# Kernel tuning notes

Measured on AMD Instinct MI355X. Metric: run time of the kernel, lower is better.

Reference implementation:

```python
import jax, jax.numpy as jnp
import numpy as np

NUM_HEADS = 8


def _forward(x, Wq, bq, Wk, bk, Wv, bv, Wo, bo, w1, b1, w2, b2, tau):
    B, S, E = x.shape
    H = NUM_HEADS
    hd = E // H
    scale = hd ** -0.5

    def heads(t):
        return t.reshape(B, S, H, hd).transpose(0, 2, 1, 3)  # [B,H,S,hd]

    q = heads(x @ Wq + bq)
    k = heads(x @ Wk + bk)
    v = heads(x @ Wv + bv)
    s = jnp.einsum('bhqd,bhkd->bhqk', q, k) * scale  # [B,H,S,S]

    # ---- autopoietic transform (vectorized over batch, no mask) ----
    s = jnp.clip(jnp.nan_to_num(s, nan=0.0, posinf=10.0, neginf=-10.0), -15.0, 15.0)
    ma = s.mean(axis=1)  # mean over heads -> [B,S,S]
    eps_safe = 0.05  # clamp(eps=1e-6, 0.05, 0.8)
    sa = jnp.clip(jnp.clip(ma, -8.0, 8.0) * eps_safe, -10.0, 10.0)
    # 1x1 conv on [1,1,S,S] == per-channel scalar scale+bias -> [B,C,S,S]
    hid = jax.nn.relu(jnp.clip(sa[:, None] * w1[None, :, None, None]
                               + b1[None, :, None, None], -5.0, 5.0))
    ap = jnp.clip(jnp.einsum('bcij,c->bij', hid, w2) + b2, -5.0, 5.0)
    taylor = jnp.clip(1.0 + 0.05 * (ap * 50.0), 0.5, 1.5)
    sig = jax.nn.sigmoid(taylor)
    p = jax.nn.softmax(jnp.clip(ma, -10.0, 10.0), axis=-1)
    Hent = -p * jnp.log(p + 1e-6)
    Fm = jax.nn.softmax(3.0 * Hent, axis=-1)
    t = sig * Fm
    eo = jnp.sqrt((ma * ma).sum(axis=(1, 2), keepdims=True)) + 1e-4  # fro norm
    et = jnp.sqrt((t * t).sum(axis=(1, 2), keepdims=True)) + 1e-4
    t = jnp.clip(eo / et, 0.8, 1.2) * t
    tm = t.mean(axis=(1, 2), keepdims=True)
    om = ma.mean(axis=(1, 2), keepdims=True)
    tstd = jnp.sqrt(jnp.clip(((t - tm) ** 2).mean(axis=(1, 2), keepdims=True), 0.01, None))
    ostd = jnp.sqrt(jnp.clip(((ma - om) ** 2).mean(axis=(1, 2), keepdims=True), 0.01, None))
    gd = jnp.clip(ostd / tstd, 0.8, 1.2)
    ar = jnp.clip(jnp.abs(ma).max(axis=(1, 2), keepdims=True), 1.0, 10.0)
    sm = jnp.clip(0.3 / jnp.log1p(ar), 0.1, 0.5)
    st = tm + sm * gd * (t - tm)  # scaled_transform
    ent = Hent.mean(axis=(1, 2), keepdims=True)
    ne = ent / jnp.log(jnp.float32(S))  # normalized entropy (max_entropy = log S)
    rr = 0.4 * (1.0 - jnp.clip(ne, 0.0, 0.4))  # residual ratio (base 0.4, entropy-damped)
    # blend transform back into per-head scores (res_scale = 1.0)
    s = s + rr[:, None] * (st - ma)[:, None]

    attn = jax.nn.softmax(s / tau, axis=-1)
    out = jnp.einsum('bhqk,bhkd->bhqd', attn, v)
    out = out.transpose(0, 2, 1, 3).reshape(B, S, E)
    return out @ Wo + bo


def setup_inputs() -> dict:
    key = jax.random.key(0)
    ks = jax.random.split(key, 8)
    B, S, E, C = 4, 512, 512, 128
    w_scale = 0.02
    return {
        'x': jax.random.normal(ks[0], (B, S, E), dtype=jnp.float32),
        'Wq': jax.random.normal(ks[1], (E, E), dtype=jnp.float32) * w_scale,
        'bq': jnp.zeros((E,), jnp.float32),
        'Wk': jax.random.normal(ks[2], (E, E), dtype=jnp.float32) * w_scale,
        'bk': jnp.zeros((E,), jnp.float32),
        'Wv': jax.random.normal(ks[3], (E, E), dtype=jnp.float32) * w_scale,
        'bv': jnp.zeros((E,), jnp.float32),
        'Wo': jax.random.normal(ks[4], (E, E), dtype=jnp.float32) * w_scale,
        'bo': jnp.zeros((E,), jnp.float32),
        'w1': jax.random.normal(ks[5], (C,), dtype=jnp.float32) * 0.5,
        'b1': jnp.zeros((C,), jnp.float32),
        'w2': jax.random.normal(ks[6], (C,), dtype=jnp.float32) * 0.1,
        'b2': jnp.zeros((1,), jnp.float32),
        'tau': jnp.ones((1,), jnp.float32),
    }


def reference(x, Wq, bq, Wk, bk, Wv, bv, Wo, bo, w1, b1, w2, b2, tau):
    return _forward(x, Wq, bq, Wk, bk, Wv, bv, Wo, bo, w1, b1, w2, b2, tau)
```

## Files before the change

kernel.cpp:

```cpp
#include <hip/hip_runtime.h>
#include <math.h>

#define BB 4
#define SS 512
#define EE 512
#define NH 8
#define HD 64
#define NC 128
#define NTAB 4096

typedef _Float16 f16x8 __attribute__((ext_vector_type(8)));
typedef float f32x4 __attribute__((ext_vector_type(4)));

struct HL { _Float16 h, l; };

__device__ __forceinline__ float clampf(float v, float lo, float hi) {
  return fminf(fmaxf(v, lo), hi);
}
__device__ __forceinline__ HL split16(float x) {
  HL r;
  r.h = (_Float16)x;
  r.l = (_Float16)(x - (float)r.h);
  return r;
}

__device__ __forceinline__ float waveRedSum(float v) {
#pragma unroll
  for (int o = 32; o; o >>= 1) v += __shfl_xor(v, o);
  return v;
}
__device__ __forceinline__ float waveRedMax(float v) {
#pragma unroll
  for (int o = 32; o; o >>= 1) v = fmaxf(v, __shfl_xor(v, o));
  return v;
}
__device__ __forceinline__ float blockRedSum(float v, float* red) {
  int tid = threadIdx.x;
  v = waveRedSum(v);
  __syncthreads();
  if ((tid & 63) == 0) red[tid >> 6] = v;
  __syncthreads();
  return red[0] + red[1] + red[2] + red[3];
}
__device__ __forceinline__ float blockRedMax(float v, float* red) {
  int tid = threadIdx.x;
  v = waveRedMax(v);
  __syncthreads();
  if ((tid & 63) == 0) red[tid >> 6] = v;
  __syncthreads();
  return fmaxf(fmaxf(red[0], red[1]), fmaxf(red[2], red[3]));
}

__global__ __launch_bounds__(256) void k_prep(
    const float* __restrict__ Wq, const float* __restrict__ Wk,
    const float* __restrict__ Wv, const float* __restrict__ Wo,
    _Float16* __restrict__ Wth, _Float16* __restrict__ Wtl) {
  const int j = blockIdx.x;
  const int tid = threadIdx.x;
  const int z = j >> 6;
  const int rem = j & 63;
  const int k0 = (rem & 7) * 64, n0 = (rem >> 3) * 64;
  const float* W = (z == 0) ? Wq : (z == 1) ? Wk : (z == 2) ? Wv : Wo;
  __shared__ float Tt[64][68];
  const int r = tid >> 2, c = (tid & 3) * 16;
#pragma unroll
  for (int jj = 0; jj < 16; jj += 4)
    *(float4*)&Tt[r][c + jj] =
        *(const float4*)(W + (size_t)(k0 + r) * EE + n0 + c + jj);
  __syncthreads();
  f16x8 h0, l0, h1, l1;
#pragma unroll
  for (int jj = 0; jj < 8; ++jj) {
    HL r0 = split16(Tt[c + jj][r]);
    HL r1 = split16(Tt[c + 8 + jj][r]);
    h0[jj] = r0.h; l0[jj] = r0.l;
    h1[jj] = r1.h; l1[jj] = r1.l;
  }
  _Float16* dh = Wth + ((size_t)z * EE + n0 + r) * EE + k0 + c;
  _Float16* dl = Wtl + ((size_t)z * EE + n0 + r) * EE + k0 + c;
  *(f16x8*)dh = h0;
  *(f16x8*)(dh + 8) = h1;
  *(f16x8*)dl = l0;
  *(f16x8*)(dl + 8) = l1;
}

__global__ __launch_bounds__(256) void k_qkv_mfma(
    const float* __restrict__ x,
    const _Float16* __restrict__ Wth, const _Float16* __restrict__ Wtl,
    const float* __restrict__ bq, const float* __restrict__ bk,
    const float* __restrict__ bv, const float* __restrict__ w1,
    const float* __restrict__ b1, const float* __restrict__ w2,
    const float* __restrict__ b2, float* __restrict__ T,
    _Float16* __restrict__ qh,
    _Float16* __restrict__ kh, _Float16* __restrict__ kl,
    _Float16* __restrict__ vth, _Float16* __restrict__ vtl) {
  const int which = blockIdx.z;
  const int tid = threadIdx.x;
  const int wave = tid >> 6, lane = tid & 63;
  const int quad = lane >> 4, l16 = lane & 15;
  const int m0 = blockIdx.y * 64;
  const int n0 = blockIdx.x * 64;
  const _Float16* Bh = Wth + (size_t)which * EE * EE;
  const _Float16* Bl = Wtl + (size_t)which * EE * EE;

  __shared__ __align__(16) char smpool[27648];
  _Float16(*LAh)[72] = (_Float16(*)[72])(smpool);
  _Float16(*LBh)[72] = (_Float16(*)[72])(smpool + 9216);
  _Float16(*LBl)[72] = (_Float16(*)[72])(smpool + 18432);
  float(*TR)[68] = (float(*)[68])(smpool);

  const int sr0 = tid >> 3, sc0 = (tid & 7) * 8;
  const int sr1 = sr0 + 32;

  float4 rx0a = *(const float4*)(x + (size_t)(m0 + sr0) * EE + sc0);
  float4 rx0b = *(const float4*)(x + (size_t)(m0 + sr0) * EE + sc0 + 4);
  float4 rx1a = *(const float4*)(x + (size_t)(m0 + sr1) * EE + sc0);
  float4 rx1b = *(const float4*)(x + (size_t)(m0 + sr1) * EE + sc0 + 4);
  f16x8 rB0h = *(const f16x8*)(Bh + (size_t)(n0 + sr0) * EE + sc0);
  f16x8 rB0l = *(const f16x8*)(Bl + (size_t)(n0 + sr0) * EE + sc0);
  f16x8 rB1h = *(const f16x8*)(Bh + (size_t)(n0 + sr1) * EE + sc0);
  f16x8 rB1l = *(const f16x8*)(Bl + (size_t)(n0 + sr1) * EE + sc0);

  f32x4 acc[4] = {};
  for (int k0 = 0; k0 < EE; k0 += 64) {
    if (k0) __syncthreads();
    {
      float f0[8] = {rx0a.x, rx0a.y, rx0a.z, rx0a.w,
                     rx0b.x, rx0b.y, rx0b.z, rx0b.w};
      float f1[8] = {rx1a.x, rx1a.y, rx1a.z, rx1a.w,
                     rx1b.x, rx1b.y, rx1b.z, rx1b.w};
      f16x8 h0, h1;
#pragma unroll
      for (int j = 0; j < 8; ++j) {
        h0[j] = (_Float16)f0[j];
        h1[j] = (_Float16)f1[j];
      }
      *(f16x8*)&LAh[sr0][sc0] = h0;
      *(f16x8*)&LAh[sr1][sc0] = h1;
    }
    *(f16x8*)&LBh[sr0][sc0] = rB0h;
    *(f16x8*)&LBl[sr0][sc0] = rB0l;
    *(f16x8*)&LBh[sr1][sc0] = rB1h;
    *(f16x8*)&LBl[sr1][sc0] = rB1l;
    __syncthreads();
    if (k0 + 64 < EE) {
      const int kn = k0 + 64;
      rx0a = *(const float4*)(x + (size_t)(m0 + sr0) * EE + kn + sc0);
      rx0b = *(const float4*)(x + (size_t)(m0 + sr0) * EE + kn + sc0 + 4);
      rx1a = *(const float4*)(x + (size_t)(m0 + sr1) * EE + kn + sc0);
      rx1b = *(const float4*)(x + (size_t)(m0 + sr1) * EE + kn + sc0 + 4);
      rB0h = *(const f16x8*)(Bh + (size_t)(n0 + sr0) * EE + kn + sc0);
      rB0l = *(const f16x8*)(Bl + (size_t)(n0 + sr0) * EE + kn + sc0);
      rB1h = *(const f16x8*)(Bh + (size_t)(n0 + sr1) * EE + kn + sc0);
      rB1l = *(const f16x8*)(Bl + (size_t)(n0 + sr1) * EE + kn + sc0);
    }
#pragma unroll
    for (int kk = 0; kk < 64; kk += 32) {
      f16x8 ah = *(const f16x8*)&LAh[wave * 16 + l16][kk + quad * 8];
#pragma unroll
      for (int nt = 0; nt < 4; ++nt) {
        f16x8 bhf = *(const f16x8*)&LBh[nt * 16 + l16][kk + quad * 8];
        f16x8 blf = *(const f16x8*)&LBl[nt * 16 + l16][kk + quad * 8];
        acc[nt] = __builtin_amdgcn_mfma_f32_16x16x32_f16(ah, bhf, acc[nt], 0, 0, 0);
        acc[nt] = __builtin_amdgcn_mfma_f32_16x16x32_f16(ah, blf, acc[nt], 0, 0, 0);
      }
    }
  }
  const float* bias = (which == 0) ? bq : (which == 1) ? bk : bv;
  if (which == 2) {
    __syncthreads();
#pragma unroll
    for (int nt = 0; nt < 4; ++nt) {
      const int dcol = nt * 16 + l16;
      const float bb = bias[n0 + nt * 16 + l16];
#pragma unroll
      for (int r = 0; r < 4; ++r)
        TR[dcol][wave * 16 + quad * 4 + r] = acc[nt][r] + bb;
    }
    __syncthreads();
    const int d = tid >> 2, cc = (tid & 3) * 16;
    const int bh = (m0 >> 9) * NH + (n0 >> 6);
    const int si0 = m0 & 511;
    f16x8 h0, l0, h1, l1;
#pragma unroll
    for (int jj = 0; jj < 8; ++jj) {
      HL r0 = split16(TR[d][cc + jj]);
      HL r1 = split16(TR[d][cc + 8 + jj]);
      h0[jj] = r0.h; l0[jj] = r0.l;
      h1[jj] = r1.h; l1[jj] = r1.l;
    }
    _Float16* dh = vth + ((size_t)bh * HD + d) * SS + si0 + cc;
    _Float16* dl = vtl + ((size_t)bh * HD + d) * SS + si0 + cc;
    *(f16x8*)dh = h0;
    *(f16x8*)(dh + 8) = h1;
    *(f16x8*)dl = l0;
    *(f16x8*)(dl + 8) = l1;
  } else {
    const float postscale = (which == 0) ? 0.125f : 1.0f;
    const int mbase = m0 + wave * 16 + quad * 4;
#pragma unroll
    for (int nt = 0; nt < 4; ++nt) {
      const int col = n0 + nt * 16 + l16;
      const float bb = bias[col];
#pragma unroll
      for (int r = 0; r < 4; ++r) {
        const size_t idx = (size_t)(mbase + r) * EE + col;
        const float val = (acc[nt][r] + bb) * postscale;
        if (which == 0) {
          qh[idx] = (_Float16)val;
        } else {
          HL sp = split16(val);
          kh[idx] = sp.h;
          kl[idx] = sp.l;
        }
      }
    }
    if (which == 0 && blockIdx.x == 0 && blockIdx.y < 17) {
      int idx = blockIdx.y * 256 + tid;
      if (idx <= NTAB) {
        float sa = -0.4f + (float)idx * (0.8f / (float)NTAB);
        float ap = 0.f;
#pragma unroll 4
        for (int c = 0; c < NC; ++c) {
          float h = fminf(fmaxf(sa * w1[c] + b1[c], 0.f), 5.f);
          ap += h * w2[c];
        }
        ap = clampf(ap + b2[0], -5.f, 5.f);
        float tay = clampf(1.0f + 0.05f * (ap * 50.0f), 0.5f, 1.5f);
        T[idx] = 1.0f / (1.0f + expf(-tay));
      }
    }
  }
}

__global__ __launch_bounds__(256) void k_ma_mfma(
    const _Float16* __restrict__ qh,
    const _Float16* __restrict__ kh, const _Float16* __restrict__ kl,
    float* __restrict__ ma) {
  const int tid = threadIdx.x;
  const int wave = tid >> 6, lane = tid & 63;
  const int quad = lane >> 4, l16 = lane & 15;
  const int m0 = blockIdx.y * 64;
  const int n0 = blockIdx.x * 64;
  const _Float16* Bh = kh + (size_t)(m0 >> 9) * SS * EE;
  const _Float16* Bl = kl + (size_t)(m0 >> 9) * SS * EE;

  __shared__ _Float16 LAh[64][72], LBh[64][72], LBl[64][72];

  const int sr0 = tid >> 3, sc0 = (tid & 7) * 8;
  const int sr1 = sr0 + 32;

  f16x8 rA0h = *(const f16x8*)(qh + (size_t)(m0 + sr0) * EE + sc0);
  f16x8 rB0h = *(const f16x8*)(Bh + (size_t)(n0 + sr0) * EE + sc0);
  f16x8 rB0l = *(const f16x8*)(Bl + (size_t)(n0 + sr0) * EE + sc0);
  f16x8 rA1h = *(const f16x8*)(qh + (size_t)(m0 + sr1) * EE + sc0);
  f16x8 rB1h = *(const f16x8*)(Bh + (size_t)(n0 + sr1) * EE + sc0);
  f16x8 rB1l = *(const f16x8*)(Bl + (size_t)(n0 + sr1) * EE + sc0);

  f32x4 acc[4] = {};
  for (int k0 = 0; k0 < EE; k0 += 64) {
    if (k0) __syncthreads();
    *(f16x8*)&LAh[sr0][sc0] = rA0h;
    *(f16x8*)&LBh[sr0][sc0] = rB0h;
    *(f16x8*)&LBl[sr0][sc0] = rB0l;
    *(f16x8*)&LAh[sr1][sc0] = rA1h;
    *(f16x8*)&LBh[sr1][sc0] = rB1h;
    *(f16x8*)&LBl[sr1][sc0] = rB1l;
    __syncthreads();
    if (k0 + 64 < EE) {
      const int kn = k0 + 64;
      rA0h = *(const f16x8*)(qh + (size_t)(m0 + sr0) * EE + kn + sc0);
      rB0h = *(const f16x8*)(Bh + (size_t)(n0 + sr0) * EE + kn + sc0);
      rB0l = *(const f16x8*)(Bl + (size_t)(n0 + sr0) * EE + kn + sc0);
      rA1h = *(const f16x8*)(qh + (size_t)(m0 + sr1) * EE + kn + sc0);
      rB1h = *(const f16x8*)(Bh + (size_t)(n0 + sr1) * EE + kn + sc0);
      rB1l = *(const f16x8*)(Bl + (size_t)(n0 + sr1) * EE + kn + sc0);
    }
#pragma unroll
    for (int kk = 0; kk < 64; kk += 32) {
      f16x8 ah = *(const f16x8*)&LAh[wave * 16 + l16][kk + quad * 8];
#pragma unroll
      for (int nt = 0; nt < 4; ++nt) {
        f16x8 bhf = *(const f16x8*)&LBh[nt * 16 + l16][kk + quad * 8];
        f16x8 blf = *(const f16x8*)&LBl[nt * 16 + l16][kk + quad * 8];
        acc[nt] = __builtin_amdgcn_mfma_f32_16x16x32_f16(ah, bhf, acc[nt], 0, 0, 0);
        acc[nt] = __builtin_amdgcn_mfma_f32_16x16x32_f16(ah, blf, acc[nt], 0, 0, 0);
      }
    }
  }
  const int mbase = m0 + wave * 16 + quad * 4;
#pragma unroll
  for (int nt = 0; nt < 4; ++nt) {
    const int col = n0 + nt * 16 + l16;
#pragma unroll
    for (int r = 0; r < 4; ++r) {
      ma[(size_t)(mbase + r) * SS + col] = acc[nt][r] * 0.125f;
    }
  }
}

__global__ __launch_bounds__(256) void k_rowstat(
    const float* __restrict__ ma, const float* __restrict__ T,
    float* __restrict__ t_un, float* __restrict__ rowred) {
  const int row = blockIdx.x * 4 + (threadIdx.x >> 6);
  const int lane = threadIdx.x & 63;

  const float4* p =
      reinterpret_cast<const float4*>(ma + (size_t)row * SS) + lane * 2;
  float4 u0 = p[0], u1 = p[1];
  float m[8] = {u0.x, u0.y, u0.z, u0.w, u1.x, u1.y, u1.z, u1.w};

  float sma = 0.f, sma2 = 0.f, mabs = 0.f;
#pragma unroll
  for (int e = 0; e < 8; ++e) {
    sma += m[e];
    sma2 += m[e] * m[e];
    mabs = fmaxf(mabs, fabsf(m[e]));
  }
  sma = waveRedSum(sma);
  sma2 = waveRedSum(sma2);
  mabs = waveRedMax(mabs);

  float ex[8], esum = 0.f;
#pragma unroll
  for (int e = 0; e < 8; ++e) {
    ex[e] = expf(clampf(m[e], -10.f, 10.f));
    esum += ex[e];
  }
  esum = waveRedSum(esum);
  float inv = 1.0f / esum;
  float Hv[8], sH = 0.f;
#pragma unroll
  for (int e = 0; e < 8; ++e) {
    float pp = ex[e] * inv;
    Hv[e] = -pp * logf(pp + 1e-6f);
    sH += Hv[e];
  }
  sH = waveRedSum(sH);

  float fx[8], fsum = 0.f;
#pragma unroll
  for (int e = 0; e < 8; ++e) {
    fx[e] = expf(3.0f * Hv[e]);
    fsum += fx[e];
  }
  fsum = waveRedSum(fsum);
  float finv = 1.0f / fsum;

  float t[8], st = 0.f, st2 = 0.f;
#pragma unroll
  for (int e = 0; e < 8; ++e) {
    float sa = clampf(m[e], -8.f, 8.f) * 0.05f;
    float pos = (sa + 0.4f) * ((float)NTAB / 0.8f);
    int idx = (int)pos;
    idx = idx < 0 ? 0 : (idx > NTAB - 1 ? NTAB - 1 : idx);
    float frac = pos - (float)idx;
    float g0 = T[idx], g1 = T[idx + 1];
    float sig = g0 + (g1 - g0) * frac;
    t[e] = sig * fx[e] * finv;
    st += t[e];
    st2 += t[e] * t[e];
  }
  st = waveRedSum(st);
  st2 = waveRedSum(st2);
  {
    float4* tp = reinterpret_cast<float4*>(t_un + (size_t)row * SS) + lane * 2;
    float4 w0 = {t[0], t[1], t[2], t[3]}, w1v = {t[4], t[5], t[6], t[7]};
    tp[0] = w0;
    tp[1] = w1v;
  }
  if (lane == 0) {
    float* rp = rowred + (size_t)row * 8;
    rp[0] = sma; rp[1] = sma2; rp[2] = mabs;
    rp[3] = st;  rp[4] = st2;  rp[5] = sH;
  }
}

__global__ __launch_bounds__(256) void k_av_fused(
    const _Float16* __restrict__ qh,
    const _Float16* __restrict__ kh, const _Float16* __restrict__ kl,
    const float* __restrict__ ma, const float* __restrict__ t_un,
    const float* __restrict__ rowred, const float* __restrict__ tau,
    const _Float16* __restrict__ vth, const _Float16* __restrict__ vtl,
    _Float16* __restrict__ oh) {
  const int bh = blockIdx.y;
  const int b_ = bh >> 3, hh = bh & 7;
  const int m0 = blockIdx.x * 32;
  const int tid = threadIdx.x;
  const int wave = tid >> 6, lane = tid & 63;
  const int quad = lane >> 4, l16 = lane & 15;
  const int mt = wave >> 1, nt = wave & 1;

  __shared__ float red[4];
  float c0, c1, c2;
  {
    const float* r0 = rowred + ((size_t)b_ * SS + tid * 2) * 8;
    const float* r1 = r0 + 8;
    float sma = blockRedSum(r0[0] + r1[0], red);
    float sma2 = blockRedSum(r0[1] + r1[1], red);
    float mabs = blockRedMax(fmaxf(r0[2], r1[2]), red);
    float st = blockRedSum(r0[3] + r1[3], red);
    float st2 = blockRedSum(r0[4] + r1[4], red);
    float sH = blockRedSum(r0[5] + r1[5], red);
    const float N = (float)(SS * SS);
    float eo = sqrtf(sma2) + 1e-4f;
    float et = sqrtf(st2) + 1e-4f;
    float r = clampf(eo / et, 0.8f, 1.2f);
    float tmean = r * st / N;
    float om = sma / N;
    float vart = r * r * fmaxf(st2 / N - (st / N) * (st / N), 0.f);
    float tstd = sqrtf(fmaxf(vart, 0.01f));
    float varo = fmaxf(sma2 / N - om * om, 0.f);
    float ostd = sqrtf(fmaxf(varo, 0.01f));
    float gd = clampf(ostd / tstd, 0.8f, 1.2f);
    float ar = clampf(mabs, 1.f, 10.f);
    float sm = clampf(0.3f / log1pf(ar), 0.1f, 0.5f);
    float ent = sH / N;
    float ne = ent / logf((float)SS);
    float rr = 0.4f * (1.f - clampf(ne, 0.f, 0.4f));
    float G = sm * gd;
    c0 = rr * (1.f - G) * tmean;
    c1 = rr * G * r;
    c2 = rr;
  }
  const float itau = 1.0f / tau[0];

  __shared__ _Float16 Ph[32][40];
  __shared__ float Zp[32][2];

  const size_t qbase = (size_t)(b_ * SS + m0 + mt * 16 + l16) * EE + hh * HD;
  f16x8 a_hi[2];
#pragma unroll
  for (int ks = 0; ks < 2; ++ks)
    a_hi[ks] = *(const f16x8*)(qh + qbase + ks * 32 + quad * 8);

  const size_t kbase = (size_t)b_ * SS * EE + hh * HD;
  const size_t vbase = ((size_t)bh * HD + wave * 16 + l16) * SS;
  const size_t mbase =
      (size_t)(b_ * SS + m0 + mt * 16 + quad * 4) * SS + nt * 16 + l16;

  f16x8 kb_h[2], kb_l[2], vb_h, vb_l;
  float mv[4], tv[4];
  {
    const size_t kr = kbase + (size_t)(nt * 16 + l16) * EE;
#pragma unroll
    for (int ks = 0; ks < 2; ++ks) {
      kb_h[ks] = *(const f16x8*)(kh + kr + ks * 32 + quad * 8);
      kb_l[ks] = *(const f16x8*)(kl + kr + ks * 32 + quad * 8);
    }
    vb_h = *(const f16x8*)(vth + vbase + quad * 8);
    vb_l = *(const f16x8*)(vtl + vbase + quad * 8);
#pragma unroll
    for (int r = 0; r < 4; ++r) {
      mv[r] = ma[mbase + (size_t)r * SS];
      tv[r] = t_un[mbase + (size_t)r * SS];
    }
  }

  float z[4] = {0.f, 0.f, 0.f, 0.f};
  f32x4 oacc[2] = {};
  for (int k0 = 0; k0 < SS; k0 += 32) {
    f32x4 qacc = {};
#pragma unroll
    for (int ks = 0; ks < 2; ++ks) {
      qacc = __builtin_amdgcn_mfma_f32_16x16x32_f16(a_hi[ks], kb_h[ks], qacc, 0, 0, 0);
      qacc = __builtin_amdgcn_mfma_f32_16x16x32_f16(a_hi[ks], kb_l[ks], qacc, 0, 0, 0);
    }
    const f16x8 vh_c = vb_h, vl_c = vb_l;
    __syncthreads();
#pragma unroll
    for (int r = 0; r < 4; ++r) {
      float sc = clampf(qacc[r], -15.f, 15.f);
      float v = (sc + c0 + c1 * tv[r] - c2 * mv[r]) * itau;
      float e = expf(v) * 1.52587890625e-05f;
      z[r] += e;
      Ph[mt * 16 + quad * 4 + r][nt * 16 + l16] = (_Float16)e;
    }
    if (k0 + 32 < SS) {
      const int kn = k0 + 32;
      const size_t kr = kbase + (size_t)(kn + nt * 16 + l16) * EE;
#pragma unroll
      for (int ks = 0; ks < 2; ++ks) {
        kb_h[ks] = *(const f16x8*)(kh + kr + ks * 32 + quad * 8);
        kb_l[ks] = *(const f16x8*)(kl + kr + ks * 32 + quad * 8);
      }
      vb_h = *(const f16x8*)(vth + vbase + kn + quad * 8);
      vb_l = *(const f16x8*)(vtl + vbase + kn + quad * 8);
#pragma unroll
      for (int r = 0; r < 4; ++r) {
        mv[r] = ma[mbase + (size_t)r * SS + kn];
        tv[r] = t_un[mbase + (size_t)r * SS + kn];
      }
    }
    __syncthreads();
#pragma unroll
    for (int mt2 = 0; mt2 < 2; ++mt2) {
      f16x8 ah = *(const f16x8*)&Ph[mt2 * 16 + l16][quad * 8];
      oacc[mt2] = __builtin_amdgcn_mfma_f32_16x16x32_f16(ah, vh_c, oacc[mt2], 0, 0, 0);
      oacc[mt2] = __builtin_amdgcn_mfma_f32_16x16x32_f16(ah, vl_c, oacc[mt2], 0, 0, 0);
    }
  }
#pragma unroll
  for (int off = 1; off < 16; off <<= 1) {
#pragma unroll
    for (int r = 0; r < 4; ++r) z[r] += __shfl_xor(z[r], off);
  }
  if (l16 == 0) {
#pragma unroll
    for (int r = 0; r < 4; ++r) Zp[mt * 16 + quad * 4 + r][nt] = z[r];
  }
  __syncthreads();
#pragma unroll
  for (int mt2 = 0; mt2 < 2; ++mt2) {
#pragma unroll
    for (int r = 0; r < 4; ++r) {
      const int lr = mt2 * 16 + quad * 4 + r;
      const float Z = Zp[lr][0] + Zp[lr][1];
      const float oV = oacc[mt2][r] / Z;
      const int si = m0 + lr;
      const size_t idx =
          ((size_t)(b_ * SS + si)) * EE + hh * HD + wave * 16 + l16;
      oh[idx] = (_Float16)oV;
    }
  }
}

__global__ __launch_bounds__(256) void k_out_mfma(
    const _Float16* __restrict__ oh,
    const _Float16* __restrict__ Wth, const _Float16* __restrict__ Wtl,
    const float* __restrict__ bo, float* __restrict__ out) {
  const int tid = threadIdx.x;
  const int wave = tid >> 6, lane = tid & 63;
  const int quad = lane >> 4, l16 = lane & 15;
  const int m0 = blockIdx.y * 64;
  const int n0 = blockIdx.x * 64;
  const _Float16* Bh = Wth + (size_t)3 * EE * EE;
  const _Float16* Bl = Wtl + (size_t)3 * EE * EE;

  __shared__ _Float16 LAh[64][72], LBh[64][72], LBl[64][72];

  const int sr0 = tid >> 3, sc0 = (tid & 7) * 8;
  const int sr1 = sr0 + 32;

  f16x8 rA0h = *(const f16x8*)(oh + (size_t)(m0 + sr0) * EE + sc0);
  f16x8 rB0h = *(const f16x8*)(Bh + (size_t)(n0 + sr0) * EE + sc0);
  f16x8 rB0l = *(const f16x8*)(Bl + (size_t)(n0 + sr0) * EE + sc0);
  f16x8 rA1h = *(const f16x8*)(oh + (size_t)(m0 + sr1) * EE + sc0);
  f16x8 rB1h = *(const f16x8*)(Bh + (size_t)(n0 + sr1) * EE + sc0);
  f16x8 rB1l = *(const f16x8*)(Bl + (size_t)(n0 + sr1) * EE + sc0);

  f32x4 acc[4] = {};
  for (int k0 = 0; k0 < EE; k0 += 64) {
    if (k0) __syncthreads();
    *(f16x8*)&LAh[sr0][sc0] = rA0h;
    *(f16x8*)&LBh[sr0][sc0] = rB0h;
    *(f16x8*)&LBl[sr0][sc0] = rB0l;
    *(f16x8*)&LAh[sr1][sc0] = rA1h;
    *(f16x8*)&LBh[sr1][sc0] = rB1h;
    *(f16x8*)&LBl[sr1][sc0] = rB1l;
    __syncthreads();
    if (k0 + 64 < EE) {
      const int kn = k0 + 64;
      rA0h = *(const f16x8*)(oh + (size_t)(m0 + sr0) * EE + kn + sc0);
      rB0h = *(const f16x8*)(Bh + (size_t)(n0 + sr0) * EE + kn + sc0);
      rB0l = *(const f16x8*)(Bl + (size_t)(n0 + sr0) * EE + kn + sc0);
      rA1h = *(const f16x8*)(oh + (size_t)(m0 + sr1) * EE + kn + sc0);
      rB1h = *(const f16x8*)(Bh + (size_t)(n0 + sr1) * EE + kn + sc0);
      rB1l = *(const f16x8*)(Bl + (size_t)(n0 + sr1) * EE + kn + sc0);
    }
#pragma unroll
    for (int kk = 0; kk < 64; kk += 32) {
      f16x8 ah = *(const f16x8*)&LAh[wave * 16 + l16][kk + quad * 8];
#pragma unroll
      for (int nt = 0; nt < 4; ++nt) {
        f16x8 bhf = *(const f16x8*)&LBh[nt * 16 + l16][kk + quad * 8];
        f16x8 blf = *(const f16x8*)&LBl[nt * 16 + l16][kk + quad * 8];
        acc[nt] = __builtin_amdgcn_mfma_f32_16x16x32_f16(ah, bhf, acc[nt], 0, 0, 0);
        acc[nt] = __builtin_amdgcn_mfma_f32_16x16x32_f16(ah, blf, acc[nt], 0, 0, 0);
      }
    }
  }
  const int mbase = m0 + wave * 16 + quad * 4;
#pragma unroll
  for (int nt = 0; nt < 4; ++nt) {
    const int col = n0 + nt * 16 + l16;
    const float bb = bo[col];
#pragma unroll
    for (int r = 0; r < 4; ++r) {
      const int m = mbase + r;
      out[(size_t)m * EE + col] = acc[nt][r] + bb;
    }
  }
}

extern "C" void kernel_launch(void* const* d_in, const int* in_sizes, int n_in,
                              void* d_out, int out_size, void* d_ws,
                              size_t ws_size, hipStream_t stream) {
  const float* x = (const float*)d_in[0];
  const float* Wq = (const float*)d_in[1];
  const float* bq = (const float*)d_in[2];
  const float* Wk = (const float*)d_in[3];
  const float* bk = (const float*)d_in[4];
  const float* Wv = (const float*)d_in[5];
  const float* bv = (const float*)d_in[6];
  const float* Wo = (const float*)d_in[7];
  const float* bo = (const float*)d_in[8];
  const float* w1 = (const float*)d_in[9];
  const float* b1 = (const float*)d_in[10];
  const float* w2 = (const float*)d_in[11];
  const float* b2 = (const float*)d_in[12];
  const float* tau = (const float*)d_in[13];
  float* out = (float*)d_out;

  const size_t NX = (size_t)2048 * EE;
  const size_t NW = (size_t)4 * EE * EE;
  const size_t NQK = (size_t)BB * SS * EE;

  _Float16* Wth = (_Float16*)d_ws;
  _Float16* Wtl = Wth + NW;
  _Float16* qh = Wtl + NW;
  _Float16* kh = qh + NQK;
  _Float16* kl = kh + NQK;
  _Float16* vth = kl + NQK;
  _Float16* vtl = vth + NQK;
  _Float16* oh = vtl + NQK;
  float* ma = (float*)(oh + NX);
  float* t_un = ma + (size_t)BB * SS * SS;
  float* T = t_un + (size_t)BB * SS * SS;
  float* rowred = T + 8192;

  k_prep<<<256, 256, 0, stream>>>(Wq, Wk, Wv, Wo, Wth, Wtl);
  k_qkv_mfma<<<dim3(8, 32, 3), 256, 0, stream>>>(x, Wth, Wtl, bq, bk, bv, w1,
                                                 b1, w2, b2, T, qh, kh, kl,
                                                 vth, vtl);
  k_ma_mfma<<<dim3(8, 32), 256, 0, stream>>>(qh, kh, kl, ma);
  k_rowstat<<<512, 256, 0, stream>>>(ma, T, t_un, rowred);
  k_av_fused<<<dim3(16, 32), 256, 0, stream>>>(qh, kh, kl, ma, t_un,
                                               rowred, tau, vth, vtl, oh);
  k_out_mfma<<<dim3(8, 32), 256, 0, stream>>>(oh, Wth, Wtl, bo, out);
}
```

Baseline: 158.1 us.

## Store ma/t_un in fp16, pre-convert x, enlarge attention tiles, use fast math

Several changes land together. The head-mean score matrix and the unnormalized transform are now stored as fp16 instead of fp32, which halves the S×S traffic between the ma, rowstat and attention kernels. x is converted to fp16 once in the prep kernel so the QKV GEMM no longer converts it in its inner loop. The fused attention kernel moves to 512-thread blocks covering 64 query rows each, which halves the K/V reloads per row, and expf/logf become the fast intrinsics. The cost is lower precision in ma, t_un and the softmax terms, plus an extra pass over x.

Result: slower. 165.1 us (+4.4%).

```diff
diff --git a/kernel.cpp b/kernel.cpp
--- a/kernel.cpp
+++ b/kernel.cpp
@@ -34,29 +34,56 @@
   for (int o = 32; o; o >>= 1) v = fmaxf(v, __shfl_xor(v, o));
   return v;
 }
-__device__ __forceinline__ float blockRedSum(float v, float* red) {
+__device__ __forceinline__ float blockRedSum8(float v, float* red) {
   int tid = threadIdx.x;
   v = waveRedSum(v);
   __syncthreads();
   if ((tid & 63) == 0) red[tid >> 6] = v;
   __syncthreads();
-  return red[0] + red[1] + red[2] + red[3];
-}
-__device__ __forceinline__ float blockRedMax(float v, float* red) {
+  float s = 0.f;
+#pragma unroll
+  for (int i = 0; i < 8; ++i) s += red[i];
+  return s;
+}
+__device__ __forceinline__ float blockRedMax8(float v, float* red) {
   int tid = threadIdx.x;
   v = waveRedMax(v);
   __syncthreads();
   if ((tid & 63) == 0) red[tid >> 6] = v;
   __syncthreads();
-  return fmaxf(fmaxf(red[0], red[1]), fmaxf(red[2], red[3]));
+  float s = red[0];
+#pragma unroll
+  for (int i = 1; i < 8; ++i) s = fmaxf(s, red[i]);
+  return s;
 }
 
 __global__ __launch_bounds__(256) void k_prep(
     const float* __restrict__ Wq, const float* __restrict__ Wk,
     const float* __restrict__ Wv, const float* __restrict__ Wo,
-    _Float16* __restrict__ Wth, _Float16* __restrict__ Wtl) {
+    const float* __restrict__ x,
+    _Float16* __restrict__ Wth, _Float16* __restrict__ Wtl,
+    _Float16* __restrict__ xh) {
   const int j = blockIdx.x;
   const int tid = threadIdx.x;
+  if (j >= 256) {
+    const int rb = (j - 256) * 64;
+    const int r = tid >> 2;
+    const int c0 = (tid & 3) * 128;
+    const float* src = x + (size_t)(rb + r) * EE + c0;
+    _Float16* dst = xh + (size_t)(rb + r) * EE + c0;
+#pragma unroll
+    for (int c = 0; c < 128; c += 8) {
+      float4 a = *(const float4*)(src + c);
+      float4 b = *(const float4*)(src + c + 4);
+      f16x8 h;
+      h[0] = (_Float16)a.x; h[1] = (_Float16)a.y;
+      h[2] = (_Float16)a.z; h[3] = (_Float16)a.w;
+      h[4] = (_Float16)b.x; h[5] = (_Float16)b.y;
+      h[6] = (_Float16)b.z; h[7] = (_Float16)b.w;
+      *(f16x8*)(dst + c) = h;
+    }
+    return;
+  }
   const int z = j >> 6;
   const int rem = j & 63;
   const int k0 = (rem & 7) * 64, n0 = (rem >> 3) * 64;
@@ -85,7 +112,7 @@
 }
 
 __global__ __launch_bounds__(256) void k_qkv_mfma(
-    const float* __restrict__ x,
+    const _Float16* __restrict__ xh,
     const _Float16* __restrict__ Wth, const _Float16* __restrict__ Wtl,
     const float* __restrict__ bq, const float* __restrict__ bk,
     const float* __restrict__ bv, const float* __restrict__ w1,
@@ -112,10 +139,8 @@
   const int sr0 = tid >> 3, sc0 = (tid & 7) * 8;
   const int sr1 = sr0 + 32;
 
-  float4 rx0a = *(const float4*)(x + (size_t)(m0 + sr0) * EE + sc0);
-  float4 rx0b = *(const float4*)(x + (size_t)(m0 + sr0) * EE + sc0 + 4);
-  float4 rx1a = *(const float4*)(x + (size_t)(m0 + sr1) * EE + sc0);
-  float4 rx1b = *(const float4*)(x + (size_t)(m0 + sr1) * EE + sc0 + 4);
+  f16x8 rA0h = *(const f16x8*)(xh + (size_t)(m0 + sr0) * EE + sc0);
+  f16x8 rA1h = *(const f16x8*)(xh + (size_t)(m0 + sr1) * EE + sc0);
   f16x8 rB0h = *(const f16x8*)(Bh + (size_t)(n0 + sr0) * EE + sc0);
   f16x8 rB0l = *(const f16x8*)(Bl + (size_t)(n0 + sr0) * EE + sc0);
   f16x8 rB1h = *(const f16x8*)(Bh + (size_t)(n0 + sr1) * EE + sc0);
@@ -124,20 +149,8 @@
   f32x4 acc[4] = {};
   for (int k0 = 0; k0 < EE; k0 += 64) {
     if (k0) __syncthreads();
-    {
-      float f0[8] = {rx0a.x, rx0a.y, rx0a.z, rx0a.w,
-                     rx0b.x, rx0b.y, rx0b.z, rx0b.w};
-      float f1[8] = {rx1a.x, rx1a.y, rx1a.z, rx1a.w,
-                     rx1b.x, rx1b.y, rx1b.z, rx1b.w};
-      f16x8 h0, h1;
-#pragma unroll
-      for (int j = 0; j < 8; ++j) {
-        h0[j] = (_Float16)f0[j];
-        h1[j] = (_Float16)f1[j];
-      }
-      *(f16x8*)&LAh[sr0][sc0] = h0;
-      *(f16x8*)&LAh[sr1][sc0] = h1;
-    }
+    *(f16x8*)&LAh[sr0][sc0] = rA0h;
+    *(f16x8*)&LAh[sr1][sc0] = rA1h;
     *(f16x8*)&LBh[sr0][sc0] = rB0h;
     *(f16x8*)&LBl[sr0][sc0] = rB0l;
     *(f16x8*)&LBh[sr1][sc0] = rB1h;
@@ -145,10 +158,8 @@
     __syncthreads();
     if (k0 + 64 < EE) {
       const int kn = k0 + 64;
-      rx0a = *(const float4*)(x + (size_t)(m0 + sr0) * EE + kn + sc0);
-      rx0b = *(const float4*)(x + (size_t)(m0 + sr0) * EE + kn + sc0 + 4);
-      rx1a = *(const float4*)(x + (size_t)(m0 + sr1) * EE + kn + sc0);
-      rx1b = *(const float4*)(x + (size_t)(m0 + sr1) * EE + kn + sc0 + 4);
+      rA0h = *(const f16x8*)(xh + (size_t)(m0 + sr0) * EE + kn + sc0);
+      rA1h = *(const f16x8*)(xh + (size_t)(m0 + sr1) * EE + kn + sc0);
       rB0h = *(const f16x8*)(Bh + (size_t)(n0 + sr0) * EE + kn + sc0);
       rB0l = *(const f16x8*)(Bl + (size_t)(n0 + sr0) * EE + kn + sc0);
       rB1h = *(const f16x8*)(Bh + (size_t)(n0 + sr1) * EE + kn + sc0);
@@ -236,7 +247,7 @@
 __global__ __launch_bounds__(256) void k_ma_mfma(
     const _Float16* __restrict__ qh,
     const _Float16* __restrict__ kh, const _Float16* __restrict__ kl,
-    float* __restrict__ ma) {
+    _Float16* __restrict__ ma) {
   const int tid = threadIdx.x;
   const int wave = tid >> 6, lane = tid & 63;
   const int quad = lane >> 4, l16 = lane & 15;
@@ -294,21 +305,21 @@
     const int col = n0 + nt * 16 + l16;
 #pragma unroll
     for (int r = 0; r < 4; ++r) {
-      ma[(size_t)(mbase + r) * SS + col] = acc[nt][r] * 0.125f;
+      ma[(size_t)(mbase + r) * SS + col] = (_Float16)(acc[nt][r] * 0.125f);
     }
   }
 }
 
 __global__ __launch_bounds__(256) void k_rowstat(
-    const float* __restrict__ ma, const float* __restrict__ T,
-    float* __restrict__ t_un, float* __restrict__ rowred) {
+    const _Float16* __restrict__ ma, const float* __restrict__ T,
+    _Float16* __restrict__ t_un, float* __restrict__ rowred) {
   const int row = blockIdx.x * 4 + (threadIdx.x >> 6);
   const int lane = threadIdx.x & 63;
 
-  const float4* p =
-      reinterpret_cast<const float4*>(ma + (size_t)row * SS) + lane * 2;
-  float4 u0 = p[0], u1 = p[1];
-  float m[8] = {u0.x, u0.y, u0.z, u0.w, u1.x, u1.y, u1.z, u1.w};
+  f16x8 mv8 = *(const f16x8*)(ma + (size_t)row * SS + lane * 8);
+  float m[8];
+#pragma unroll
+  for (int e = 0; e < 8; ++e) m[e] = (float)mv8[e];
 
   float sma = 0.f, sma2 = 0.f, mabs = 0.f;
 #pragma unroll
@@ -324,7 +335,7 @@
   float ex[8], esum = 0.f;
 #pragma unroll
   for (int e = 0; e < 8; ++e) {
-    ex[e] = expf(clampf(m[e], -10.f, 10.f));
+    ex[e] = __expf(clampf(m[e], -10.f, 10.f));
     esum += ex[e];
   }
   esum = waveRedSum(esum);
@@ -333,7 +344,7 @@
 #pragma unroll
   for (int e = 0; e < 8; ++e) {
     float pp = ex[e] * inv;
-    Hv[e] = -pp * logf(pp + 1e-6f);
+    Hv[e] = -pp * __logf(pp + 1e-6f);
     sH += Hv[e];
   }
   sH = waveRedSum(sH);
@@ -341,7 +352,7 @@
   float fx[8], fsum = 0.f;
 #pragma unroll
   for (int e = 0; e < 8; ++e) {
-    fx[e] = expf(3.0f * Hv[e]);
+    fx[e] = __expf(3.0f * Hv[e]);
     fsum += fx[e];
   }
   fsum = waveRedSum(fsum);
@@ -364,10 +375,10 @@
   st = waveRedSum(st);
   st2 = waveRedSum(st2);
   {
-    float4* tp = reinterpret_cast<float4*>(t_un + (size_t)row * SS) + lane * 2;
-    float4 w0 = {t[0], t[1], t[2], t[3]}, w1v = {t[4], t[5], t[6], t[7]};
-    tp[0] = w0;
-    tp[1] = w1v;
+    f16x8 tw;
+#pragma unroll
+    for (int e = 0; e < 8; ++e) tw[e] = (_Float16)t[e];
+    *(f16x8*)(t_un + (size_t)row * SS + lane * 8) = tw;
   }
   if (lane == 0) {
     float* rp = rowred + (size_t)row * 8;
@@ -376,32 +387,31 @@
   }
 }
 
-__global__ __launch_bounds__(256) void k_av_fused(
+__global__ __launch_bounds__(512) void k_av_fused(
     const _Float16* __restrict__ qh,
     const _Float16* __restrict__ kh, const _Float16* __restrict__ kl,
-    const float* __restrict__ ma, const float* __restrict__ t_un,
+    const _Float16* __restrict__ ma, const _Float16* __restrict__ t_un,
     const float* __restrict__ rowred, const float* __restrict__ tau,
     const _Float16* __restrict__ vth, const _Float16* __restrict__ vtl,
     _Float16* __restrict__ oh) {
   const int bh = blockIdx.y;
   const int b_ = bh >> 3, hh = bh & 7;
-  const int m0 = blockIdx.x * 32;
+  const int m0 = blockIdx.x * 64;
   const int tid = threadIdx.x;
   const int wave = tid >> 6, lane = tid & 63;
   const int quad = lane >> 4, l16 = lane & 15;
-  const int mt = wave >> 1, nt = wave & 1;
-
-  __shared__ float red[4];
+  const int g = wave >> 1, h2 = wave & 1;
+
+  __shared__ float red[8];
   float c0, c1, c2;
   {
-    const float* r0 = rowred + ((size_t)b_ * SS + tid * 2) * 8;
-    const float* r1 = r0 + 8;
-    float sma = blockRedSum(r0[0] + r1[0], red);
-    float sma2 = blockRedSum(r0[1] + r1[1], red);
-    float mabs = blockRedMax(fmaxf(r0[2], r1[2]), red);
-    float st = blockRedSum(r0[3] + r1[3], red);
-    float st2 = blockRedSum(r0[4] + r1[4], red);
-    float sH = blockRedSum(r0[5] + r1[5], red);
+    const float* rp = rowred + ((size_t)b_ * SS + tid) * 8;
+    float sma = blockRedSum8(rp[0], red);
+    float sma2 = blockRedSum8(rp[1], red);
+    float mabs = blockRedMax8(rp[2], red);
+    float st = blockRedSum8(rp[3], red);
+    float st2 = blockRedSum8(rp[4], red);
+    float sH = blockRedSum8(rp[5], red);
     const float N = (float)(SS * SS);
     float eo = sqrtf(sma2) + 1e-4f;
     float et = sqrtf(st2) + 1e-4f;
@@ -425,24 +435,24 @@
   }
   const float itau = 1.0f / tau[0];
 
-  __shared__ _Float16 Ph[32][40];
-  __shared__ float Zp[32][2];
-
-  const size_t qbase = (size_t)(b_ * SS + m0 + mt * 16 + l16) * EE + hh * HD;
+  __shared__ _Float16 Ph[64][40];
+  __shared__ float Zp[64][2];
+
+  const size_t qbase = (size_t)(b_ * SS + m0 + g * 16 + l16) * EE + hh * HD;
   f16x8 a_hi[2];
 #pragma unroll
   for (int ks = 0; ks < 2; ++ks)
     a_hi[ks] = *(const f16x8*)(qh + qbase + ks * 32 + quad * 8);
 
   const size_t kbase = (size_t)b_ * SS * EE + hh * HD;
-  const size_t vbase = ((size_t)bh * HD + wave * 16 + l16) * SS;
-  const size_t mbase =
-      (size_t)(b_ * SS + m0 + mt * 16 + quad * 4) * SS + nt * 16 + l16;
+  const size_t vbase = ((size_t)bh * HD + g * 16 + l16) * SS;
+  const size_t mb0 =
+      (size_t)(b_ * SS + m0 + g * 16 + quad * 4) * SS + h2 * 16 + l16;
 
   f16x8 kb_h[2], kb_l[2], vb_h, vb_l;
-  float mv[4], tv[4];
+  _Float16 mv[4], tv[4];
   {
-    const size_t kr = kbase + (size_t)(nt * 16 + l16) * EE;
+    const size_t kr = kbase + (size_t)(h2 * 16 + l16) * EE;
 #pragma unroll
     for (int ks = 0; ks < 2; ++ks) {
       kb_h[ks] = *(const f16x8*)(kh + kr + ks * 32 + quad * 8);
@@ -452,8 +462,8 @@
     vb_l = *(const f16x8*)(vtl + vbase + quad * 8);
 #pragma unroll
     for (int r = 0; r < 4; ++r) {
-      mv[r] = ma[mbase + (size_t)r * SS];
-      tv[r] = t_un[mbase + (size_t)r * SS];
+      mv[r] = ma[mb0 + (size_t)r * SS];
+      tv[r] = t_un[mb0 + (size_t)r * SS];
     }
   }
 
@@ -471,14 +481,14 @@
 #pragma unroll
     for (int r = 0; r < 4; ++r) {
       float sc = clampf(qacc[r], -15.f, 15.f);
-      float v = (sc + c0 + c1 * tv[r] - c2 * mv[r]) * itau;
-      float e = expf(v) * 1.52587890625e-05f;
+      float v = (sc + c0 + c1 * (float)tv[r] - c2 * (float)mv[r]) * itau;
+      float e = __expf(v) * 1.52587890625e-05f;
       z[r] += e;
-      Ph[mt * 16 + quad * 4 + r][nt * 16 + l16] = (_Float16)e;
+      Ph[g * 16 + quad * 4 + r][h2 * 16 + l16] = (_Float16)e;
     }
     if (k0 + 32 < SS) {
       const int kn = k0 + 32;
-      const size_t kr = kbase + (size_t)(kn + nt * 16 + l16) * EE;
+      const size_t kr = kbase + (size_t)(kn + h2 * 16 + l16) * EE;
 #pragma unroll
       for (int ks = 0; ks < 2; ++ks) {
         kb_h[ks] = *(const f16x8*)(kh + kr + ks * 32 + quad * 8);
@@ -488,16 +498,17 @@
       vb_l = *(const f16x8*)(vtl + vbase + kn + quad * 8);
 #pragma unroll
       for (int r = 0; r < 4; ++r) {
-        mv[r] = ma[mbase + (size_t)r * SS + kn];
-        tv[r] = t_un[mbase + (size_t)r * SS + kn];
+        mv[r] = ma[mb0 + (size_t)r * SS + kn];
+        tv[r] = t_un[mb0 + (size_t)r * SS + kn];
       }
     }
     __syncthreads();
 #pragma unroll
-    for (int mt2 = 0; mt2 < 2; ++mt2) {
+    for (int e2 = 0; e2 < 2; ++e2) {
+      const int mt2 = h2 * 2 + e2;
       f16x8 ah = *(const f16x8*)&Ph[mt2 * 16 + l16][quad * 8];
-      oacc[mt2] = __builtin_amdgcn_mfma_f32_16x16x32_f16(ah, vh_c, oacc[mt2], 0, 0, 0);
-      oacc[mt2] = __builtin_amdgcn_mfma_f32_16x16x32_f16(ah, vl_c, oacc[mt2], 0, 0, 0);
+      oacc[e2] = __builtin_amdgcn_mfma_f32_16x16x32_f16(ah, vh_c, oacc[e2], 0, 0, 0);
+      oacc[e2] = __builtin_amdgcn_mfma_f32_16x16x32_f16(ah, vl_c, oacc[e2], 0, 0, 0);
     }
   }
 #pragma unroll
@@ -507,19 +518,20 @@
   }
   if (l16 == 0) {
 #pragma unroll
-    for (int r = 0; r < 4; ++r) Zp[mt * 16 + quad * 4 + r][nt] = z[r];
+    for (int r = 0; r < 4; ++r) Zp[g * 16 + quad * 4 + r][h2] = z[r];
   }
   __syncthreads();
 #pragma unroll
-  for (int mt2 = 0; mt2 < 2; ++mt2) {
+  for (int e2 = 0; e2 < 2; ++e2) {
+    const int mt2 = h2 * 2 + e2;
 #pragma unroll
     for (int r = 0; r < 4; ++r) {
       const int lr = mt2 * 16 + quad * 4 + r;
       const float Z = Zp[lr][0] + Zp[lr][1];
-      const float oV = oacc[mt2][r] / Z;
+      const float oV = oacc[e2][r] / Z;
       const int si = m0 + lr;
       const size_t idx =
-          ((size_t)(b_ * SS + si)) * EE + hh * HD + wave * 16 + l16;
+          ((size_t)(b_ * SS + si)) * EE + hh * HD + g * 16 + l16;
       oh[idx] = (_Float16)oV;
     }
   }
@@ -615,27 +627,29 @@
   const size_t NX = (size_t)2048 * EE;
   const size_t NW = (size_t)4 * EE * EE;
   const size_t NQK = (size_t)BB * SS * EE;
+  const size_t NSS = (size_t)BB * SS * SS;
 
   _Float16* Wth = (_Float16*)d_ws;
   _Float16* Wtl = Wth + NW;
-  _Float16* qh = Wtl + NW;
+  _Float16* xh = Wtl + NW;
+  _Float16* qh = xh + NX;
   _Float16* kh = qh + NQK;
   _Float16* kl = kh + NQK;
   _Float16* vth = kl + NQK;
   _Float16* vtl = vth + NQK;
   _Float16* oh = vtl + NQK;
-  float* ma = (float*)(oh + NX);
-  float* t_un = ma + (size_t)BB * SS * SS;
-  float* T = t_un + (size_t)BB * SS * SS;
+  _Float16* ma = oh + NX;
+  _Float16* t_un = ma + NSS;
+  float* T = (float*)(t_un + NSS);
   float* rowred = T + 8192;
 
-  k_prep<<<256, 256, 0, stream>>>(Wq, Wk, Wv, Wo, Wth, Wtl);
-  k_qkv_mfma<<<dim3(8, 32, 3), 256, 0, stream>>>(x, Wth, Wtl, bq, bk, bv, w1,
+  k_prep<<<288, 256, 0, stream>>>(Wq, Wk, Wv, Wo, x, Wth, Wtl, xh);
+  k_qkv_mfma<<<dim3(8, 32, 3), 256, 0, stream>>>(xh, Wth, Wtl, bq, bk, bv, w1,
                                                  b1, w2, b2, T, qh, kh, kl,
                                                  vth, vtl);
   k_ma_mfma<<<dim3(8, 32), 256, 0, stream>>>(qh, kh, kl, ma);
   k_rowstat<<<512, 256, 0, stream>>>(ma, T, t_un, rowred);
-  k_av_fused<<<dim3(16, 32), 256, 0, stream>>>(qh, kh, kl, ma, t_un,
-                                               rowred, tau, vth, vtl, oh);
+  k_av_fused<<<dim3(8, 32), 512, 0, stream>>>(qh, kh, kl, ma, t_un,
+                                              rowred, tau, vth, vtl, oh);
   k_out_mfma<<<dim3(8, 32), 256, 0, stream>>>(oh, Wth, Wtl, bo, out);
 }
```
